# Optimization experiments

Hardware: AMD Instinct MI355X
Metric: run time of the kernel (lower is better)

The kernel has to match this reference:

```python
import jax, jax.numpy as jnp
import numpy as np

EMB = 768
HS = 64
B, T = 4, 4096


def setup_inputs() -> dict:
    key = jax.random.key(0)
    ks = jax.random.split(key, 7)
    s = 1.0 / np.sqrt(EMB)
    return {
        "x": jax.random.normal(ks[0], (B, T, EMB), dtype=jnp.float32),
        "Wk": jax.random.normal(ks[1], (EMB, HS), dtype=jnp.float32) * s,
        "bk": jnp.zeros((HS,), dtype=jnp.float32),
        "Wq": jax.random.normal(ks[2], (EMB, HS), dtype=jnp.float32) * s,
        "bq": jnp.zeros((HS,), dtype=jnp.float32),
        "Wv": jax.random.normal(ks[3], (EMB, HS), dtype=jnp.float32) * s,
        "bv": jnp.zeros((HS,), dtype=jnp.float32),
    }


def reference(x, Wk, bk, Wq, bq, Wv, bv):
    # Linear projections: (B, T, emb) @ (emb, hs) + bias -> (B, T, hs)
    k = x @ Wk + bk
    q = x @ Wq + bq
    v = x @ Wv + bv
    # NOTE: original code computes key @ query^T (k on the left), no 1/sqrt(hs) scaling.
    att = jnp.einsum("bth,bsh->bts", k, q)  # (B, T, T)
    causal = jnp.tril(jnp.ones((T, T), dtype=bool))  # (T, T)
    att = jnp.where(causal, att, -jnp.inf)
    wei = jax.nn.softmax(att, axis=-1)
    return jnp.einsum("bts,bsh->bth", wei, v)  # (B, T, hs)
```

## Files before the change

kernel.cpp:

```cpp
#include <hip/hip_runtime.h>
#include <cmath>

static constexpr int EMB  = 768;
static constexpr int HS   = 64;
static constexpr int NB   = 4;
static constexpr int SEQ  = 4096;
static constexpr int MTOT = NB * SEQ;

typedef __attribute__((ext_vector_type(8))) short  short8x;
typedef __attribute__((ext_vector_type(4))) float  float4x;
typedef __attribute__((ext_vector_type(4))) unsigned short ushort4x;

__device__ inline unsigned short rne16(float f) {
    unsigned u = __builtin_bit_cast(unsigned, f);
    unsigned r = u + 0x7FFFu + ((u >> 16) & 1u);
    return (unsigned short)(r >> 16);
}
__device__ inline float bf2f(unsigned short h) {
    return __builtin_bit_cast(float, ((unsigned)h) << 16);
}

__global__ __launch_bounds__(256) void convert_w(
    const float* __restrict__ Wk, const float* __restrict__ Wq, const float* __restrict__ Wv,
    unsigned short* __restrict__ wpk)
{
    const int t    = blockIdx.x * 256 + threadIdx.x;
    const int lane = t & 63;
    const int rest = t >> 6;
    const int nng  = rest % 12;
    const int kcp  = rest / 12;
    const int kc   = kcp % 24;
    const int p    = kcp / 24;
    const int which= nng >> 2;
    const int nn   = nng & 3;
    const float* W = (which == 0) ? Wk : (which == 1) ? Wq : Wv;
    const int col  = nn * 16 + (lane & 15);
    const int kr   = kc * 32 + (lane >> 4) * 8;

    unsigned short o[8];
    #pragma unroll
    for (int j = 0; j < 8; ++j) {
        float w = W[(size_t)(kr + j) * HS + col];
        unsigned short h = rne16(w);
        o[j] = (p == 0) ? h : rne16(w - bf2f(h));
    }
    size_t base = ((size_t)((p * 24 + kc) * 12 + nng) * 64 + lane) * 8;
    *(short8x*)&wpk[base] = *(short8x*)o;
}

__global__ __launch_bounds__(256) void proj_kernel(
    const float* __restrict__ x,
    const unsigned short* __restrict__ wpk,
    const float* __restrict__ bk, const float* __restrict__ bq, const float* __restrict__ bv,
    unsigned short* __restrict__ khi, unsigned short* __restrict__ klo,
    unsigned short* __restrict__ qhi, unsigned short* __restrict__ qlo,
    unsigned short* __restrict__ vT)
{
    __shared__ unsigned short xh[2][32 * 72];
    __shared__ unsigned short xl[2][32 * 72];

    const int tid  = threadIdx.x;
    const int lane = tid & 63;
    const int w    = tid >> 6;
    const int l15  = lane & 15;
    const int quad = lane >> 4;
    const int row0 = blockIdx.x * 32;

    float4x acc[3][2] = {};
    float4  pre[2];

    const int s_r  = tid >> 4;
    const int s_c4 = (tid & 15) * 4;

    #pragma unroll
    for (int it = 0; it < 2; ++it) {
        const int fi = tid + it * 256;
        const int r  = fi >> 4, c4 = (fi & 15) * 4;
        pre[it] = *(const float4*)&x[(size_t)(row0 + r) * EMB + 0 * 64 + c4];
    }
    #pragma unroll
    for (int it = 0; it < 2; ++it) {
        const int fi = tid + it * 256;
        const int r  = fi >> 4, c4 = (fi & 15) * 4;
        const float4 xv = pre[it];
        const unsigned short h0 = rne16(xv.x), h1 = rne16(xv.y),
                             h2 = rne16(xv.z), h3 = rne16(xv.w);
        ushort4x hv = {h0, h1, h2, h3};
        ushort4x lv = {rne16(xv.x - bf2f(h0)), rne16(xv.y - bf2f(h1)),
                       rne16(xv.z - bf2f(h2)), rne16(xv.w - bf2f(h3))};
        *(ushort4x*)&xh[0][r * 72 + c4] = hv;
        *(ushort4x*)&xl[0][r * 72 + c4] = lv;
    }

    for (int ch = 0; ch < 12; ++ch) {
        if (ch + 1 < 12) {
            #pragma unroll
            for (int it = 0; it < 2; ++it) {
                const int fi = tid + it * 256;
                const int r  = fi >> 4, c4 = (fi & 15) * 4;
                pre[it] = *(const float4*)&x[(size_t)(row0 + r) * EMB + (ch + 1) * 64 + c4];
            }
        }
        __syncthreads();
        const int buf = ch & 1;

        #pragma unroll
        for (int k0i = 0; k0i < 2; ++k0i) {
            const int k0 = k0i * 32;
            const int kc = ch * 2 + k0i;
            short8x ah[2], al[2];
            #pragma unroll
            for (int mi = 0; mi < 2; ++mi) {
                ah[mi] = *(const short8x*)&xh[buf][(mi * 16 + l15) * 72 + k0 + quad * 8];
                al[mi] = *(const short8x*)&xl[buf][(mi * 16 + l15) * 72 + k0 + quad * 8];
            }
            #pragma unroll
            for (int which = 0; which < 3; ++which) {
                const int nng = which * 4 + w;
                const short8x bh = *(const short8x*)&wpk[((size_t)((0 * 24 + kc) * 12 + nng) * 64 + lane) * 8];
                const short8x bl = *(const short8x*)&wpk[((size_t)((1 * 24 + kc) * 12 + nng) * 64 + lane) * 8];
                #pragma unroll
                for (int mi = 0; mi < 2; ++mi) {
                    acc[which][mi] = __builtin_amdgcn_mfma_f32_16x16x32_bf16(ah[mi], bh, acc[which][mi], 0, 0, 0);
                    acc[which][mi] = __builtin_amdgcn_mfma_f32_16x16x32_bf16(ah[mi], bl, acc[which][mi], 0, 0, 0);
                    acc[which][mi] = __builtin_amdgcn_mfma_f32_16x16x32_bf16(al[mi], bh, acc[which][mi], 0, 0, 0);
                }
            }
        }

        if (ch + 1 < 12) {
            const int nbuf = (ch + 1) & 1;
            #pragma unroll
            for (int it = 0; it < 2; ++it) {
                const int fi = tid + it * 256;
                const int r  = fi >> 4, c4 = (fi & 15) * 4;
                const float4 xv = pre[it];
                const unsigned short h0 = rne16(xv.x), h1 = rne16(xv.y),
                                     h2 = rne16(xv.z), h3 = rne16(xv.w);
                ushort4x hv = {h0, h1, h2, h3};
                ushort4x lv = {rne16(xv.x - bf2f(h0)), rne16(xv.y - bf2f(h1)),
                               rne16(xv.z - bf2f(h2)), rne16(xv.w - bf2f(h3))};
                *(ushort4x*)&xh[nbuf][r * 72 + c4] = hv;
                *(ushort4x*)&xl[nbuf][r * 72 + c4] = lv;
            }
        }
    }

    const int col = w * 16 + l15;
    const float bkv = bk[col], bqv = bq[col], bvv = bv[col];
    #pragma unroll
    for (int mi = 0; mi < 2; ++mi) {
        const int rbase = row0 + mi * 16 + quad * 4;
        #pragma unroll
        for (int r = 0; r < 4; ++r) {
            const float kv = acc[0][mi][r] + bkv;
            const unsigned short hk = rne16(kv);
            khi[(size_t)(rbase + r) * 64 + col] = hk;
            klo[(size_t)(rbase + r) * 64 + col] = rne16(kv - bf2f(hk));
            const float qv = acc[1][mi][r] + bqv;
            const unsigned short hq = rne16(qv);
            qhi[(size_t)(rbase + r) * 64 + col] = hq;
            qlo[(size_t)(rbase + r) * 64 + col] = rne16(qv - bf2f(hq));
        }
        const int b = rbase / SEQ;
        const int s = rbase % SEQ;
        ushort4x vv = {rne16(acc[2][mi][0] + bvv), rne16(acc[2][mi][1] + bvv),
                       rne16(acc[2][mi][2] + bvv), rne16(acc[2][mi][3] + bvv)};
        *(ushort4x*)&vT[((size_t)b * 64 + col) * SEQ + s] = vv;
    }
}

__global__ __launch_bounds__(256) void attn_kernel(
    const unsigned short* __restrict__ khi, const unsigned short* __restrict__ klo,
    const unsigned short* __restrict__ qhi, const unsigned short* __restrict__ qlo,
    const unsigned short* __restrict__ vT,
    float* __restrict__ Opart, float* __restrict__ lpart, int SPLITS)
{
    __shared__ unsigned short kh_s[64 * 72];
    __shared__ unsigned short kl_s[64 * 72];
    __shared__ unsigned short vt_s[64 * 72];
    __shared__ unsigned short ps[64 * 72];

    const int tid  = threadIdx.x;
    const int lane = tid & 63;
    const int w    = tid >> 6;
    const int l15  = lane & 15;
    const int quad = lane >> 4;

    const int n    = blockIdx.x;
    const int sp   = n % SPLITS;
    const int rest = n / SPLITS;
    const int b    = rest % NB;
    const int j    = rest / NB;
    const int t0   = j * 64;
    const size_t rowb = (size_t)b * SEQ;

    const int qrow = t0 + 16 * w + l15;
    short8x qa_h[2], qa_l[2];
    #pragma unroll
    for (int k0 = 0; k0 < 2; ++k0) {
        qa_h[k0] = *(const short8x*)&khi[(rowb + qrow) * 64 + k0 * 32 + quad * 8];
        qa_l[k0] = *(const short8x*)&klo[(rowb + qrow) * 64 + k0 * 32 + quad * 8];
    }

    float l_r[4] = {0.f, 0.f, 0.f, 0.f};
    float4x oacc[4] = {};

    const int sr = tid >> 3;
    const int c8 = (tid & 7) * 8;

    for (int ci = sp; ci <= j; ci += SPLITS) {
        const int s0 = ci * 64;
        __syncthreads();
        #pragma unroll
        for (int it = 0; it < 2; ++it) {
            const int r = sr + it * 32;
            *(short8x*)&kh_s[r * 72 + c8] = *(const short8x*)&qhi[(rowb + s0 + r) * 64 + c8];
            *(short8x*)&kl_s[r * 72 + c8] = *(const short8x*)&qlo[(rowb + s0 + r) * 64 + c8];
            *(short8x*)&vt_s[r * 72 + c8] = *(const short8x*)&vT[((size_t)b * 64 + r) * SEQ + s0 + c8];
        }
        __syncthreads();

        float4x sacc[4] = {};
        #pragma unroll
        for (int k0 = 0; k0 < 2; ++k0) {
            #pragma unroll
            for (int nn = 0; nn < 4; ++nn) {
                const short8x bh = *(const short8x*)&kh_s[(nn * 16 + l15) * 72 + k0 * 32 + quad * 8];
                const short8x bl = *(const short8x*)&kl_s[(nn * 16 + l15) * 72 + k0 * 32 + quad * 8];
                sacc[nn] = __builtin_amdgcn_mfma_f32_16x16x32_bf16(qa_h[k0], bh, sacc[nn], 0, 0, 0);
                sacc[nn] = __builtin_amdgcn_mfma_f32_16x16x32_bf16(qa_h[k0], bl, sacc[nn], 0, 0, 0);
                sacc[nn] = __builtin_amdgcn_mfma_f32_16x16x32_bf16(qa_l[k0], bh, sacc[nn], 0, 0, 0);
            }
        }

        if (ci == j) {
            const int trow = t0 + 16 * w + quad * 4;
            #pragma unroll
            for (int nn = 0; nn < 4; ++nn) {
                const int colg = s0 + nn * 16 + l15;
                #pragma unroll
                for (int r = 0; r < 4; ++r)
                    if (colg > trow + r) sacc[nn][r] = -1e30f;
            }
        }

        #pragma unroll
        for (int nn = 0; nn < 4; ++nn) {
            #pragma unroll
            for (int r = 0; r < 4; ++r) {
                const float e = __expf(fminf(sacc[nn][r], 80.0f));
                const unsigned short h = rne16(e);
                l_r[r] += bf2f(h);
                ps[(16 * w + quad * 4 + r) * 72 + nn * 16 + l15] = h;
            }
        }
        __syncthreads();

        #pragma unroll
        for (int k0 = 0; k0 < 2; ++k0) {
            const short8x pa = *(const short8x*)&ps[(16 * w + l15) * 72 + k0 * 32 + quad * 8];
            #pragma unroll
            for (int nn = 0; nn < 4; ++nn) {
                const short8x vb = *(const short8x*)&vt_s[(nn * 16 + l15) * 72 + k0 * 32 + quad * 8];
                oacc[nn] = __builtin_amdgcn_mfma_f32_16x16x32_bf16(pa, vb, oacc[nn], 0, 0, 0);
            }
        }
    }

    #pragma unroll
    for (int r = 0; r < 4; ++r) {
        l_r[r] += __shfl_xor(l_r[r], 1);
        l_r[r] += __shfl_xor(l_r[r], 2);
        l_r[r] += __shfl_xor(l_r[r], 4);
        l_r[r] += __shfl_xor(l_r[r], 8);
    }
    const size_t part = (size_t)(j * NB + b) * SPLITS + sp;
    float* Op = Opart + part * 4096;
    #pragma unroll
    for (int nn = 0; nn < 4; ++nn)
        #pragma unroll
        for (int r = 0; r < 4; ++r)
            Op[(16 * w + quad * 4 + r) * 64 + nn * 16 + l15] = oacc[nn][r];
    if (l15 == 0) {
        #pragma unroll
        for (int r = 0; r < 4; ++r)
            lpart[part * 64 + 16 * w + quad * 4 + r] = l_r[r];
    }
}

__global__ __launch_bounds__(256) void combine_kernel(
    const float* __restrict__ Opart, const float* __restrict__ lpart,
    float* __restrict__ out, int SPLITS)
{
    const int j   = blockIdx.x;
    const int b   = blockIdx.y;
    const int tid = threadIdx.x;
    const int row = tid >> 2;
    const int c0  = (tid & 3) * 16;
    const size_t base = (size_t)(j * NB + b) * SPLITS;

    float4 acc[4] = {};
    float l = 0.f;
    for (int sp = 0; sp < SPLITS; ++sp) {
        const float* Op = Opart + (base + sp) * 4096;
        #pragma unroll
        for (int u = 0; u < 4; ++u) {
            const float4 v = *(const float4*)&Op[row * 64 + c0 + u * 4];
            acc[u].x += v.x; acc[u].y += v.y; acc[u].z += v.z; acc[u].w += v.w;
        }
        l += lpart[(base + sp) * 64 + row];
    }
    const float inv = 1.0f / l;
    float* o = out + ((size_t)b * SEQ + j * 64 + row) * 64 + c0;
    #pragma unroll
    for (int u = 0; u < 4; ++u) {
        float4 v;
        v.x = acc[u].x * inv; v.y = acc[u].y * inv;
        v.z = acc[u].z * inv; v.w = acc[u].w * inv;
        *(float4*)&o[u * 4] = v;
    }
}

extern "C" void kernel_launch(void* const* d_in, const int* in_sizes, int n_in,
                              void* d_out, int out_size, void* d_ws, size_t ws_size,
                              hipStream_t stream)
{
    const float* x  = (const float*)d_in[0];
    const float* Wk = (const float*)d_in[1];
    const float* bk = (const float*)d_in[2];
    const float* Wq = (const float*)d_in[3];
    const float* bq = (const float*)d_in[4];
    const float* Wv = (const float*)d_in[5];
    const float* bv = (const float*)d_in[6];
    float* out = (float*)d_out;

    const size_t NE = (size_t)MTOT * HS;
    unsigned short* khi = (unsigned short*)d_ws;
    unsigned short* klo = khi + NE;
    unsigned short* qhi = klo + NE;
    unsigned short* qlo = qhi + NE;
    unsigned short* vT  = qlo + NE;
    unsigned short* wpk = vT + NE;
    const size_t fixed_bytes = 5 * NE * sizeof(unsigned short) + 294912 * sizeof(unsigned short);

    int SPLITS = 4;
    while (SPLITS > 1) {
        const size_t need = fixed_bytes +
            (size_t)NB * 64 * SPLITS * (64 * 64 + 64) * sizeof(float);
        if (need <= ws_size) break;
        SPLITS >>= 1;
    }
    float* Opart = (float*)((char*)d_ws + fixed_bytes);
    float* lpart = Opart + (size_t)NB * 64 * SPLITS * 64 * 64;

    convert_w<<<144, 256, 0, stream>>>(Wk, Wq, Wv, wpk);
    proj_kernel<<<MTOT / 32, 256, 0, stream>>>(x, wpk, bk, bq, bv, khi, klo, qhi, qlo, vT);
    attn_kernel<<<64 * NB * SPLITS, 256, 0, stream>>>(khi, klo, qhi, qlo, vT, Opart, lpart, SPLITS);
    dim3 cgrid(64, NB);
    combine_kernel<<<cgrid, 256, 0, stream>>>(Opart, lpart, out, SPLITS);
}
```

Baseline: 169.8 us.

## Pair causal query tiles per block and accumulate splits with atomics

Each attention block now handles two query tiles, j and 63-j, so every block gets a similar amount of causal work. Each loaded K/V chunk is reused for both tiles. The split count is fixed at 8, and split results are accumulated straight into a zeroed fp32 buffer with atomicAdd. This replaces the per-split partial buffers and the multi-split combine loop, leaving an elementwise normalize kernel. It also drops one block barrier, since each wave only reads its own rows of the P tile, and adds a launch-bounds occupancy hint. The costs are a memset and atomic traffic, and the summation order is no longer deterministic.

Result: slower. 267.9 us (+57.8%).

```diff
diff --git a/kernel.cpp b/kernel.cpp
--- a/kernel.cpp
+++ b/kernel.cpp
@@ -6,6 +6,7 @@
 static constexpr int NB   = 4;
 static constexpr int SEQ  = 4096;
 static constexpr int MTOT = NB * SEQ;
+static constexpr int SPLITS = 8;
 
 typedef __attribute__((ext_vector_type(8))) short  short8x;
 typedef __attribute__((ext_vector_type(4))) float  float4x;
@@ -69,9 +70,6 @@
     float4x acc[3][2] = {};
     float4  pre[2];
 
-    const int s_r  = tid >> 4;
-    const int s_c4 = (tid & 15) * 4;
-
     #pragma unroll
     for (int it = 0; it < 2; ++it) {
         const int fi = tid + it * 256;
@@ -170,14 +168,14 @@
     }
 }
 
-__global__ __launch_bounds__(256) void attn_kernel(
+__global__ __launch_bounds__(256, 4) void attn_kernel(
     const unsigned short* __restrict__ khi, const unsigned short* __restrict__ klo,
     const unsigned short* __restrict__ qhi, const unsigned short* __restrict__ qlo,
     const unsigned short* __restrict__ vT,
-    float* __restrict__ Opart, float* __restrict__ lpart, int SPLITS)
-{
-    __shared__ unsigned short kh_s[64 * 72];
-    __shared__ unsigned short kl_s[64 * 72];
+    float* __restrict__ Oacc, float* __restrict__ lacc)
+{
+    __shared__ unsigned short qh_s[64 * 72];
+    __shared__ unsigned short ql_s[64 * 72];
     __shared__ unsigned short vt_s[64 * 72];
     __shared__ unsigned short ps[64 * 72];
 
@@ -187,55 +185,48 @@
     const int l15  = lane & 15;
     const int quad = lane >> 4;
 
-    const int n    = blockIdx.x;
-    const int sp   = n % SPLITS;
-    const int rest = n / SPLITS;
-    const int b    = rest % NB;
-    const int j    = rest / NB;
-    const int t0   = j * 64;
+    const int n  = blockIdx.x;
+    const int sp = n & (SPLITS - 1);
+    const int b  = (n >> 3) & (NB - 1);
+    const int p  = n >> 5;
+    const int jA = p, jB = 63 - p;
     const size_t rowb = (size_t)b * SEQ;
 
-    const int qrow = t0 + 16 * w + l15;
-    short8x qa_h[2], qa_l[2];
-    #pragma unroll
-    for (int k0 = 0; k0 < 2; ++k0) {
-        qa_h[k0] = *(const short8x*)&khi[(rowb + qrow) * 64 + k0 * 32 + quad * 8];
-        qa_l[k0] = *(const short8x*)&klo[(rowb + qrow) * 64 + k0 * 32 + quad * 8];
-    }
-
-    float l_r[4] = {0.f, 0.f, 0.f, 0.f};
-    float4x oacc[4] = {};
+    short8x aAh[2], aAl[2], aBh[2], aBl[2];
+    {
+        const size_t rA = rowb + jA * 64 + 16 * w + l15;
+        const size_t rB = rowb + jB * 64 + 16 * w + l15;
+        #pragma unroll
+        for (int k0 = 0; k0 < 2; ++k0) {
+            aAh[k0] = *(const short8x*)&khi[rA * 64 + k0 * 32 + quad * 8];
+            aAl[k0] = *(const short8x*)&klo[rA * 64 + k0 * 32 + quad * 8];
+            aBh[k0] = *(const short8x*)&khi[rB * 64 + k0 * 32 + quad * 8];
+            aBl[k0] = *(const short8x*)&klo[rB * 64 + k0 * 32 + quad * 8];
+        }
+    }
+
+    float lA[4] = {0.f, 0.f, 0.f, 0.f}, lB[4] = {0.f, 0.f, 0.f, 0.f};
+    float4x oA[4] = {}, oB[4] = {};
 
     const int sr = tid >> 3;
     const int c8 = (tid & 7) * 8;
 
-    for (int ci = sp; ci <= j; ci += SPLITS) {
-        const int s0 = ci * 64;
-        __syncthreads();
-        #pragma unroll
-        for (int it = 0; it < 2; ++it) {
-            const int r = sr + it * 32;
-            *(short8x*)&kh_s[r * 72 + c8] = *(const short8x*)&qhi[(rowb + s0 + r) * 64 + c8];
-            *(short8x*)&kl_s[r * 72 + c8] = *(const short8x*)&qlo[(rowb + s0 + r) * 64 + c8];
-            *(short8x*)&vt_s[r * 72 + c8] = *(const short8x*)&vT[((size_t)b * 64 + r) * SEQ + s0 + c8];
-        }
-        __syncthreads();
-
+    auto apply = [&](int j, const short8x* ah, const short8x* al,
+                     float4x* oacc, float* l_r, bool diag, int s0) {
         float4x sacc[4] = {};
         #pragma unroll
         for (int k0 = 0; k0 < 2; ++k0) {
             #pragma unroll
             for (int nn = 0; nn < 4; ++nn) {
-                const short8x bh = *(const short8x*)&kh_s[(nn * 16 + l15) * 72 + k0 * 32 + quad * 8];
-                const short8x bl = *(const short8x*)&kl_s[(nn * 16 + l15) * 72 + k0 * 32 + quad * 8];
-                sacc[nn] = __builtin_amdgcn_mfma_f32_16x16x32_bf16(qa_h[k0], bh, sacc[nn], 0, 0, 0);
-                sacc[nn] = __builtin_amdgcn_mfma_f32_16x16x32_bf16(qa_h[k0], bl, sacc[nn], 0, 0, 0);
-                sacc[nn] = __builtin_amdgcn_mfma_f32_16x16x32_bf16(qa_l[k0], bh, sacc[nn], 0, 0, 0);
-            }
-        }
-
-        if (ci == j) {
-            const int trow = t0 + 16 * w + quad * 4;
+                const short8x bh = *(const short8x*)&qh_s[(nn * 16 + l15) * 72 + k0 * 32 + quad * 8];
+                const short8x bl = *(const short8x*)&ql_s[(nn * 16 + l15) * 72 + k0 * 32 + quad * 8];
+                sacc[nn] = __builtin_amdgcn_mfma_f32_16x16x32_bf16(ah[k0], bh, sacc[nn], 0, 0, 0);
+                sacc[nn] = __builtin_amdgcn_mfma_f32_16x16x32_bf16(al[k0], bh, sacc[nn], 0, 0, 0);
+                sacc[nn] = __builtin_amdgcn_mfma_f32_16x16x32_bf16(ah[k0], bl, sacc[nn], 0, 0, 0);
+            }
+        }
+        if (diag) {
+            const int trow = j * 64 + 16 * w + quad * 4;
             #pragma unroll
             for (int nn = 0; nn < 4; ++nn) {
                 const int colg = s0 + nn * 16 + l15;
@@ -244,7 +235,6 @@
                     if (colg > trow + r) sacc[nn][r] = -1e30f;
             }
         }
-
         #pragma unroll
         for (int nn = 0; nn < 4; ++nn) {
             #pragma unroll
@@ -255,8 +245,6 @@
                 ps[(16 * w + quad * 4 + r) * 72 + nn * 16 + l15] = h;
             }
         }
-        __syncthreads();
-
         #pragma unroll
         for (int k0 = 0; k0 < 2; ++k0) {
             const short8x pa = *(const short8x*)&ps[(16 * w + l15) * 72 + k0 * 32 + quad * 8];
@@ -266,60 +254,64 @@
                 oacc[nn] = __builtin_amdgcn_mfma_f32_16x16x32_bf16(pa, vb, oacc[nn], 0, 0, 0);
             }
         }
-    }
-
-    #pragma unroll
-    for (int r = 0; r < 4; ++r) {
-        l_r[r] += __shfl_xor(l_r[r], 1);
-        l_r[r] += __shfl_xor(l_r[r], 2);
-        l_r[r] += __shfl_xor(l_r[r], 4);
-        l_r[r] += __shfl_xor(l_r[r], 8);
-    }
-    const size_t part = (size_t)(j * NB + b) * SPLITS + sp;
-    float* Op = Opart + part * 4096;
-    #pragma unroll
-    for (int nn = 0; nn < 4; ++nn)
-        #pragma unroll
-        for (int r = 0; r < 4; ++r)
-            Op[(16 * w + quad * 4 + r) * 64 + nn * 16 + l15] = oacc[nn][r];
-    if (l15 == 0) {
-        #pragma unroll
-        for (int r = 0; r < 4; ++r)
-            lpart[part * 64 + 16 * w + quad * 4 + r] = l_r[r];
+    };
+
+    for (int ci = sp; ci <= jB; ci += SPLITS) {
+        const int s0 = ci * 64;
+        __syncthreads();
+        #pragma unroll
+        for (int it = 0; it < 2; ++it) {
+            const int r = sr + it * 32;
+            *(short8x*)&qh_s[r * 72 + c8] = *(const short8x*)&qhi[(rowb + s0 + r) * 64 + c8];
+            *(short8x*)&ql_s[r * 72 + c8] = *(const short8x*)&qlo[(rowb + s0 + r) * 64 + c8];
+            *(short8x*)&vt_s[r * 72 + c8] = *(const short8x*)&vT[((size_t)b * 64 + r) * SEQ + s0 + c8];
+        }
+        __syncthreads();
+
+        apply(jB, aBh, aBl, oB, lB, ci == jB, s0);
+        if (ci <= jA) apply(jA, aAh, aAl, oA, lA, ci == jA, s0);
+    }
+
+    #pragma unroll
+    for (int tile = 0; tile < 2; ++tile) {
+        float*   l_r  = tile ? lA : lB;
+        float4x* oacc = tile ? oA : oB;
+        const int j   = tile ? jA : jB;
+        if (tile && sp > jA) break;
+        #pragma unroll
+        for (int r = 0; r < 4; ++r) {
+            float l = l_r[r];
+            l += __shfl_xor(l, 1);
+            l += __shfl_xor(l, 2);
+            l += __shfl_xor(l, 4);
+            l += __shfl_xor(l, 8);
+            l_r[r] = l;
+        }
+        float* Ob = Oacc + (rowb + j * 64) * 64;
+        #pragma unroll
+        for (int nn = 0; nn < 4; ++nn)
+            #pragma unroll
+            for (int r = 0; r < 4; ++r)
+                atomicAdd(&Ob[(16 * w + quad * 4 + r) * 64 + nn * 16 + l15], oacc[nn][r]);
+        if (l15 == 0) {
+            #pragma unroll
+            for (int r = 0; r < 4; ++r)
+                atomicAdd(&lacc[rowb + j * 64 + 16 * w + quad * 4 + r], l_r[r]);
+        }
     }
 }
 
 __global__ __launch_bounds__(256) void combine_kernel(
-    const float* __restrict__ Opart, const float* __restrict__ lpart,
-    float* __restrict__ out, int SPLITS)
-{
-    const int j   = blockIdx.x;
-    const int b   = blockIdx.y;
-    const int tid = threadIdx.x;
-    const int row = tid >> 2;
-    const int c0  = (tid & 3) * 16;
-    const size_t base = (size_t)(j * NB + b) * SPLITS;
-
-    float4 acc[4] = {};
-    float l = 0.f;
-    for (int sp = 0; sp < SPLITS; ++sp) {
-        const float* Op = Opart + (base + sp) * 4096;
-        #pragma unroll
-        for (int u = 0; u < 4; ++u) {
-            const float4 v = *(const float4*)&Op[row * 64 + c0 + u * 4];
-            acc[u].x += v.x; acc[u].y += v.y; acc[u].z += v.z; acc[u].w += v.w;
-        }
-        l += lpart[(base + sp) * 64 + row];
-    }
-    const float inv = 1.0f / l;
-    float* o = out + ((size_t)b * SEQ + j * 64 + row) * 64 + c0;
-    #pragma unroll
-    for (int u = 0; u < 4; ++u) {
-        float4 v;
-        v.x = acc[u].x * inv; v.y = acc[u].y * inv;
-        v.z = acc[u].z * inv; v.w = acc[u].w * inv;
-        *(float4*)&o[u * 4] = v;
-    }
+    const float* __restrict__ Oacc, const float* __restrict__ lacc,
+    float* __restrict__ out)
+{
+    const int idx4 = blockIdx.x * 256 + threadIdx.x;
+    const int row  = idx4 >> 4;
+    const float inv = 1.0f / lacc[row];
+    const float4 v = *(const float4*)&Oacc[idx4 * 4];
+    float4 o;
+    o.x = v.x * inv; o.y = v.y * inv; o.z = v.z * inv; o.w = v.w * inv;
+    *(float4*)&out[idx4 * 4] = o;
 }
 
 extern "C" void kernel_launch(void* const* d_in, const int* in_sizes, int n_in,
@@ -342,21 +334,12 @@
     unsigned short* qlo = qhi + NE;
     unsigned short* vT  = qlo + NE;
     unsigned short* wpk = vT + NE;
-    const size_t fixed_bytes = 5 * NE * sizeof(unsigned short) + 294912 * sizeof(unsigned short);
-
-    int SPLITS = 4;
-    while (SPLITS > 1) {
-        const size_t need = fixed_bytes +
-            (size_t)NB * 64 * SPLITS * (64 * 64 + 64) * sizeof(float);
-        if (need <= ws_size) break;
-        SPLITS >>= 1;
-    }
-    float* Opart = (float*)((char*)d_ws + fixed_bytes);
-    float* lpart = Opart + (size_t)NB * 64 * SPLITS * 64 * 64;
-
+    float* Oacc = (float*)(wpk + 294912);
+    float* lacc = Oacc + NE;
+
+    hipMemsetAsync(Oacc, 0, (NE + MTOT) * sizeof(float), stream);
     convert_w<<<144, 256, 0, stream>>>(Wk, Wq, Wv, wpk);
     proj_kernel<<<MTOT / 32, 256, 0, stream>>>(x, wpk, bk, bq, bv, khi, klo, qhi, qlo, vT);
-    attn_kernel<<<64 * NB * SPLITS, 256, 0, stream>>>(khi, klo, qhi, qlo, vT, Opart, lpart, SPLITS);
-    dim3 cgrid(64, NB);
-    combine_kernel<<<cgrid, 256, 0, stream>>>(Opart, lpart, out, SPLITS);
-}
+    attn_kernel<<<32 * NB * SPLITS, 256, 0, stream>>>(khi, klo, qhi, qlo, vT, Oacc, lacc);
+    combine_kernel<<<(int)(NE / 4 / 256), 256, 0, stream>>>(Oacc, lacc, out);
+}
```
